# Kernel optimization log

Hardware: AMD Instinct MI355X
Metric: run time of the kernel (lower is better)

## Reference

```python
import jax, jax.numpy as jnp
import numpy as np
import math


def _lsq(x, s, bit, all_positive):
    # LSQ fake-quant: scale -> clamp -> round (STE) -> dequant
    if all_positive:
        qn, qp = 0.0, float(2 ** bit - 1)
    else:
        qn, qp = -float(2 ** (bit - 1)), float(2 ** (bit - 1) - 1)
    g = 1.0 / math.sqrt(x.size * qp)  # grad-scale factor (static)
    sg = s * g
    s_eff = sg + jax.lax.stop_gradient(s - sg)  # fwd = s, grad scaled by g
    xq = jnp.clip(x / s_eff, qn, qp)
    xq = xq + jax.lax.stop_gradient(jnp.round(xq) - xq)  # round with STE
    return xq * s_eff


def _conv(x, w, stride):
    return jax.lax.conv_general_dilated(
        x, w, window_strides=(stride, stride), padding='VALID',
        dimension_numbers=('NCHW', 'OIHW', 'NCHW'))


def setup_inputs() -> dict:
    key = jax.random.key(0)
    ks = jax.random.split(key, 5)
    B = 65536
    x = jax.random.normal(ks[0], (B, 1, 28, 28), dtype=jnp.float32)
    w1 = jax.random.normal(ks[1], (4, 1, 5, 5), dtype=jnp.float32) * 0.2
    w2 = jax.random.normal(ks[2], (8, 4, 3, 3), dtype=jnp.float32) * 0.2
    fc_w = jax.random.normal(ks[3], (10, 200), dtype=jnp.float32) * 0.07
    fc_b = jax.random.normal(ks[4], (10,), dtype=jnp.float32) * 0.01
    one = jnp.ones((1,), dtype=jnp.float32)
    return {"x": x, "w1": w1, "w2": w2, "fc_w": fc_w, "fc_b": fc_b,
            "s_in": one * 0.05, "s_w1": one * 0.02, "s_a1": one * 0.05,
            "s_w2": one * 0.02, "s_a2": one * 0.05, "s_fc": one * 0.02}


def reference(x, w1, w2, fc_w, fc_b, s_in, s_w1, s_a1, s_w2, s_a2, s_fc):
    x = _lsq(x, s_in, 8, False)
    x = _conv(x, _lsq(w1, s_w1, 8, False), 2)          # [B,4,12,12]
    x = jax.nn.relu(_lsq(x, s_a1, 8, True))
    x = _conv(x, _lsq(w2, s_w2, 8, False), 2)          # [B,8,5,5]
    x = jax.nn.relu(_lsq(x, s_a2, 8, True))
    x = x.reshape(x.shape[0], -1)                      # [B,200]
    return x @ _lsq(fc_w, s_fc, 8, False).T + fc_b     # [B,10]
```

## Files before the change

kernel.cpp:

```cpp
#include <hip/hip_runtime.h>
#include <math.h>

#define G  8
#define NG 8

#if __has_builtin(__builtin_amdgcn_sdot4)
__device__ __forceinline__ int dot4(unsigned a, unsigned b, int c) {
    return __builtin_amdgcn_sdot4((int)a, (int)b, c, false);
}
#else
__device__ __forceinline__ int dot4(unsigned a, unsigned b, int c) {
    c += (int)(signed char)(a & 255u)         * (int)(signed char)(b & 255u);
    c += (int)(signed char)((a >> 8) & 255u)  * (int)(signed char)((b >> 8) & 255u);
    c += (int)(signed char)((a >> 16) & 255u) * (int)(signed char)((b >> 16) & 255u);
    c += (int)(signed char)(a >> 24)          * (int)(signed char)(b >> 24);
    return c;
}
#endif

__device__ __forceinline__ float seff(float s, float gf) {
    float sg = s * gf;
    return sg + (s - sg);
}
__device__ __forceinline__ unsigned q8(float v, float s, float rs) {
    float q0 = v * rs;
    float r  = fmaf(-s, q0, v);
    float y  = fmaf(r, rs, q0);
    y = fminf(fmaxf(y, -128.f), 127.f);
    float t = y + 12582912.0f;
    return __float_as_uint(t);
}
__device__ __forceinline__ unsigned pack4(unsigned a, unsigned b, unsigned c, unsigned d) {
    return (a & 255u) | ((b & 255u) << 8) | ((c & 255u) << 16) | (d << 24);
}
__device__ __forceinline__ int mround(int acc, double r) {
    double t = fma((double)acc, r, 6755399441055744.0);
    return (int)__double_as_longlong(t);
}

extern "C" __global__ __launch_bounds__(256, 4)
void qcnn_fused(const float* __restrict__ x,  const float* __restrict__ w1,
                const float* __restrict__ w2, const float* __restrict__ fcw,
                const float* __restrict__ fcb,
                const float* __restrict__ s_in, const float* __restrict__ s_w1,
                const float* __restrict__ s_a1, const float* __restrict__ s_w2,
                const float* __restrict__ s_a2, const float* __restrict__ s_fc,
                float* __restrict__ out, int B,
                float gx, float gw1, float ga1, float gw2, float ga2, float gfc)
{
    __shared__ unsigned xs[2][G*196];
    __shared__ unsigned a1p[G*144];
    __shared__ unsigned a2p[G*50];
    __shared__ __align__(16) unsigned w1pk[4][5][4];
    __shared__ unsigned w2p[8][9];
    __shared__ unsigned fcp[10][50];
    __shared__ int K2s[8];
    __shared__ int K3s[10];
    __shared__ float fcbs[10];

    const int tid = threadIdx.x;
    const int g   = tid >> 5;
    const int t   = tid & 31;

    const float sx  = seff(s_in[0], gx);
    const float sw1 = seff(s_w1[0], gw1);
    const float sa1 = seff(s_a1[0], ga1);
    const float sw2 = seff(s_w2[0], gw2);
    const float sa2 = seff(s_a2[0], ga2);
    const float sfc = seff(s_fc[0], gfc);
    const float rsx = 1.0f / sx;
    const float rw1 = 1.0f / sw1;
    const float rw2 = 1.0f / sw2;
    const float rfc = 1.0f / sfc;
    const double r1 = (double)sx  * (double)sw1 / (double)sa1;
    const double r2 = (double)sa1 * (double)sw2 / (double)sa2;
    const double r3 = (double)sa2 * (double)sfc;

    const long long gbase = (long long)blockIdx.x * NG;

    float4 Rv0, Rv1, Rv2, Rv3, Rv4, Rv5, Rv6;
    auto stage_load = [&](long long grp) {
        const int nimg = (B - (int)(grp * G) < G) ? (B - (int)(grp * G)) : G;
        if (nimg != G) return;
        const float4* xp = (const float4*)x + grp * (long long)(G * 196);
        Rv0 = xp[tid];          Rv1 = xp[tid + 256]; Rv2 = xp[tid + 512];
        Rv3 = xp[tid + 768];    Rv4 = xp[tid + 1024];Rv5 = xp[tid + 1280];
        if (tid < 32) Rv6 = xp[tid + 1536];
    };
    auto stage_write = [&](long long grp, int buf) {
        const int nimg = (B - (int)(grp * G) < G) ? (B - (int)(grp * G)) : G;
        if (nimg <= 0) return;
        unsigned* dst = xs[buf];
        if (nimg == G) {
            float4 v;
            v = Rv0; dst[tid]        = pack4(q8(v.x,sx,rsx), q8(v.y,sx,rsx), q8(v.z,sx,rsx), q8(v.w,sx,rsx));
            v = Rv1; dst[tid + 256]  = pack4(q8(v.x,sx,rsx), q8(v.y,sx,rsx), q8(v.z,sx,rsx), q8(v.w,sx,rsx));
            v = Rv2; dst[tid + 512]  = pack4(q8(v.x,sx,rsx), q8(v.y,sx,rsx), q8(v.z,sx,rsx), q8(v.w,sx,rsx));
            v = Rv3; dst[tid + 768]  = pack4(q8(v.x,sx,rsx), q8(v.y,sx,rsx), q8(v.z,sx,rsx), q8(v.w,sx,rsx));
            v = Rv4; dst[tid + 1024] = pack4(q8(v.x,sx,rsx), q8(v.y,sx,rsx), q8(v.z,sx,rsx), q8(v.w,sx,rsx));
            v = Rv5; dst[tid + 1280] = pack4(q8(v.x,sx,rsx), q8(v.y,sx,rsx), q8(v.z,sx,rsx), q8(v.w,sx,rsx));
            if (tid < 32) {
                v = Rv6;
                dst[tid + 1536] = pack4(q8(v.x,sx,rsx), q8(v.y,sx,rsx), q8(v.z,sx,rsx), q8(v.w,sx,rsx));
            }
        } else {
            const float4* xp = (const float4*)x + grp * (long long)(G * 196);
            const int nv = nimg * 196;
            for (int i = tid; i < nv; i += 256) {
                float4 v = xp[i];
                dst[i] = pack4(q8(v.x,sx,rsx), q8(v.y,sx,rsx), q8(v.z,sx,rsx), q8(v.w,sx,rsx));
            }
        }
    };

    stage_load(gbase);

    if (tid < 80) {
        const int c = tid / 20, rem = tid % 20, ky = rem >> 2, vv = rem & 3;
        const float* wr = w1 + c*25 + ky*5;
        unsigned b[5];
        #pragma unroll
        for (int k = 0; k < 5; ++k) b[k] = q8(wr[k], sw1, rw1) & 255u;
        unsigned pk;
        if      (vv == 0) pk = b[0] | (b[1] << 8) | (b[2] << 16) | (b[3] << 24);
        else if (vv == 1) pk = b[4];
        else if (vv == 2) pk = (b[0] << 16) | (b[1] << 24);
        else              pk = b[2] | (b[3] << 8) | (b[4] << 16);
        w1pk[c][ky][vv] = pk;
    } else if (tid < 152) {
        const int d = tid - 80, oc = d / 9, tap = d % 9;
        unsigned pk = 0;
        #pragma unroll
        for (int ic = 0; ic < 4; ++ic)
            pk |= (q8(w2[oc*36 + ic*9 + tap], sw2, rw2) & 255u) << (8*ic);
        w2p[oc][tap] = pk;
    }
    if (tid < 10) fcbs[tid] = fcb[tid];
    for (int i = tid; i < 500; i += 256) {
        const int o = i / 50, kd = i % 50;
        const float* fr = fcw + o*200 + kd*4;
        unsigned pk = pack4(q8(fr[0],sfc,rfc), q8(fr[1],sfc,rfc),
                            q8(fr[2],sfc,rfc), q8(fr[3],sfc,rfc));
        fcp[o][kd] = pk;
    }
    __syncthreads();
    if (tid < 8) {
        int s = 0;
        #pragma unroll
        for (int d = 0; d < 9; ++d) s = dot4(w2p[tid][d], 0x01010101u, s);
        K2s[tid] = s << 7;
    } else if (tid < 18) {
        const int o = tid - 8;
        int s = 0;
        for (int d = 0; d < 50; ++d) s = dot4(fcp[o][d], 0x01010101u, s);
        K3s[o] = s << 7;
    }
    stage_write(gbase, 0);
    __syncthreads();

    int cur = 0;
    for (int it = 0; it < NG; ++it) {
        const long long grp = gbase + it;
        if (grp * G >= B) break;
        const int nimg = (B - (int)(grp * G) < G) ? (B - (int)(grp * G)) : G;

        if (it + 1 < NG) stage_load(grp + 1);

        if (g < nimg) {
            const int c  = t & 3;
            const int h  = (t >> 2) & 1;
            const int y0 = t >> 3;
            uint4 W[5];
            #pragma unroll
            for (int ky = 0; ky < 5; ++ky)
                W[ky] = *(const uint4*)&w1pk[c][ky][0];
            const unsigned* xb = &xs[cur][g*196];
            #pragma unroll
            for (int k = 0; k < 3; ++k) {
                const int y = y0 + 4*k;
                int acc[6] = {0,0,0,0,0,0};
                #pragma unroll
                for (int ky = 0; ky < 5; ++ky) {
                    const unsigned* rp = xb + (2*y + ky)*7 + 3*h;
                    const unsigned L0 = rp[0], L1 = rp[1], L2 = rp[2], L3 = rp[3];
                    acc[0] = dot4(L1, W[ky].y, dot4(L0, W[ky].x, acc[0]));
                    acc[1] = dot4(L1, W[ky].w, dot4(L0, W[ky].z, acc[1]));
                    acc[2] = dot4(L2, W[ky].y, dot4(L1, W[ky].x, acc[2]));
                    acc[3] = dot4(L2, W[ky].w, dot4(L1, W[ky].z, acc[3]));
                    acc[4] = dot4(L3, W[ky].y, dot4(L2, W[ky].x, acc[4]));
                    acc[5] = dot4(L3, W[ky].w, dot4(L2, W[ky].z, acc[5]));
                }
                unsigned char* dst = (unsigned char*)a1p + (g*144 + y*12 + 6*h)*4 + c;
                #pragma unroll
                for (int m = 0; m < 6; ++m) {
                    int q = mround(acc[m], r1);
                    q = min(max(q, 0), 255);
                    dst[4*m] = (unsigned char)(q - 128);
                }
            }
        }
        __syncthreads();

        for (int tau = tid; tau < G*40; tau += 256) {
            const int img = tau / 40;
            const int rem = tau - img*40;
            const int oc  = rem / 5;
            const int y   = rem - oc*5;
            if (img >= nimg) break;
            unsigned wv[9];
            #pragma unroll
            for (int d = 0; d < 9; ++d) wv[d] = w2p[oc][d];
            const int k2 = K2s[oc];
            const unsigned* base = &a1p[img*144];
            unsigned rw[3][12];
            #pragma unroll
            for (int ky = 0; ky < 3; ++ky) {
                const uint4* rp = (const uint4*)&base[(2*y + ky)*12];
                uint4 A = rp[0], Bv = rp[1], Cv = rp[2];
                rw[ky][0]=A.x;  rw[ky][1]=A.y;  rw[ky][2]=A.z;  rw[ky][3]=A.w;
                rw[ky][4]=Bv.x; rw[ky][5]=Bv.y; rw[ky][6]=Bv.z; rw[ky][7]=Bv.w;
                rw[ky][8]=Cv.x; rw[ky][9]=Cv.y; rw[ky][10]=Cv.z; rw[ky][11]=Cv.w;
            }
            unsigned char* dst = (unsigned char*)a2p + img*200 + oc*25 + y*5;
            #pragma unroll
            for (int jx = 0; jx < 5; ++jx) {
                int acc = k2;
                #pragma unroll
                for (int ky = 0; ky < 3; ++ky)
                    #pragma unroll
                    for (int kx = 0; kx < 3; ++kx)
                        acc = dot4(rw[ky][2*jx + kx], wv[ky*3 + kx], acc);
                int q = mround(acc, r2);
                q = min(max(q, 0), 255);
                dst[jx] = (unsigned char)(q - 128);
            }
        }

        if (it + 1 < NG) stage_write(grp + 1, cur ^ 1);
        __syncthreads();

        if (g < nimg && t < 30) {
            const int part = t / 10;
            const int o    = t - part*10;
            const int k0   = part * 17;
            const int nk   = (part == 2) ? 16 : 17;
            int acc = 0;
            for (int ki = 0; ki < nk; ++ki) {
                const int k = k0 + ki;
                acc = dot4(a2p[g*50 + k], fcp[o][k], acc);
            }
            const int self0 = (g & 1) * 32 + o;
            const int s1 = __shfl(acc, self0 + 10);
            const int s2 = __shfl(acc, self0 + 20);
            if (part == 0) {
                const int total = acc + s1 + s2 + K3s[o];
                const double oo = (double)total * r3 + (double)fcbs[o];
                out[(grp*G + g)*10 + o] = (float)oo;
            }
        }
        cur ^= 1;
    }
}

extern "C" void kernel_launch(void* const* d_in, const int* in_sizes, int n_in,
                              void* d_out, int out_size, void* d_ws, size_t ws_size,
                              hipStream_t stream) {
    const float* x    = (const float*)d_in[0];
    const float* w1   = (const float*)d_in[1];
    const float* w2   = (const float*)d_in[2];
    const float* fcw  = (const float*)d_in[3];
    const float* fcb  = (const float*)d_in[4];
    const float* s_in = (const float*)d_in[5];
    const float* s_w1 = (const float*)d_in[6];
    const float* s_a1 = (const float*)d_in[7];
    const float* s_w2 = (const float*)d_in[8];
    const float* s_a2 = (const float*)d_in[9];
    const float* s_fc = (const float*)d_in[10];

    const int B = in_sizes[0] / 784;
    const float gx  = (float)(1.0 / sqrt((double)B * 784.0 * 127.0));
    const float gw1 = (float)(1.0 / sqrt(100.0 * 127.0));
    const float ga1 = (float)(1.0 / sqrt((double)B * 576.0 * 255.0));
    const float gw2 = (float)(1.0 / sqrt(288.0 * 127.0));
    const float ga2 = (float)(1.0 / sqrt((double)B * 200.0 * 255.0));
    const float gfc = (float)(1.0 / sqrt(2000.0 * 127.0));

    const int imgs_per_block = G * NG;
    const int grid = (B + imgs_per_block - 1) / imgs_per_block;
    qcnn_fused<<<grid, 256, 0, stream>>>(x, w1, w2, fcw, fcb,
                                         s_in, s_w1, s_a1, s_w2, s_a2, s_fc,
                                         (float*)d_out, B,
                                         gx, gw1, ga1, gw2, ga2, gfc);
}
```

Measured before the change: 59.13 us.

## Give each image to one half-wave and replace block barriers with wave fences

The input staging and the conv2 work are remapped so that each image is handled only by its own 32-lane group. Each group loads, quantizes and stores its own image's tile. Because all data an image needs now stays inside one wavefront, the per-iteration __syncthreads calls become an inline s_waitcnt lgkmcnt(0) fence, which removes block-wide barrier stalls between stages. The risk is correctness: it relies on LDS ordering within a wave and on the compiler honouring the asm memory clobber. It also gives uneven conv2 work per lane, since only the lanes with (t&3)==0 do a second pass.

```diff
diff --git a/kernel.cpp b/kernel.cpp
--- a/kernel.cpp
+++ b/kernel.cpp
@@ -17,6 +17,10 @@
     return c;
 }
 #endif
+
+__device__ __forceinline__ void wave_fence() {
+    asm volatile("s_waitcnt lgkmcnt(0)" ::: "memory");
+}
 
 __device__ __forceinline__ float seff(float s, float gf) {
     float sg = s * gf;
@@ -80,36 +84,27 @@
 
     float4 Rv0, Rv1, Rv2, Rv3, Rv4, Rv5, Rv6;
     auto stage_load = [&](long long grp) {
-        const int nimg = (B - (int)(grp * G) < G) ? (B - (int)(grp * G)) : G;
-        if (nimg != G) return;
-        const float4* xp = (const float4*)x + grp * (long long)(G * 196);
-        Rv0 = xp[tid];          Rv1 = xp[tid + 256]; Rv2 = xp[tid + 512];
-        Rv3 = xp[tid + 768];    Rv4 = xp[tid + 1024];Rv5 = xp[tid + 1280];
-        if (tid < 32) Rv6 = xp[tid + 1536];
+        const long long img = grp * G + g;
+        if (img >= B) return;
+        const float4* xp = (const float4*)x + img * 196;
+        Rv0 = xp[t];        Rv1 = xp[t + 32];  Rv2 = xp[t + 64];
+        Rv3 = xp[t + 96];   Rv4 = xp[t + 128]; Rv5 = xp[t + 160];
+        if (t < 4) Rv6 = xp[t + 192];
     };
     auto stage_write = [&](long long grp, int buf) {
-        const int nimg = (B - (int)(grp * G) < G) ? (B - (int)(grp * G)) : G;
-        if (nimg <= 0) return;
-        unsigned* dst = xs[buf];
-        if (nimg == G) {
-            float4 v;
-            v = Rv0; dst[tid]        = pack4(q8(v.x,sx,rsx), q8(v.y,sx,rsx), q8(v.z,sx,rsx), q8(v.w,sx,rsx));
-            v = Rv1; dst[tid + 256]  = pack4(q8(v.x,sx,rsx), q8(v.y,sx,rsx), q8(v.z,sx,rsx), q8(v.w,sx,rsx));
-            v = Rv2; dst[tid + 512]  = pack4(q8(v.x,sx,rsx), q8(v.y,sx,rsx), q8(v.z,sx,rsx), q8(v.w,sx,rsx));
-            v = Rv3; dst[tid + 768]  = pack4(q8(v.x,sx,rsx), q8(v.y,sx,rsx), q8(v.z,sx,rsx), q8(v.w,sx,rsx));
-            v = Rv4; dst[tid + 1024] = pack4(q8(v.x,sx,rsx), q8(v.y,sx,rsx), q8(v.z,sx,rsx), q8(v.w,sx,rsx));
-            v = Rv5; dst[tid + 1280] = pack4(q8(v.x,sx,rsx), q8(v.y,sx,rsx), q8(v.z,sx,rsx), q8(v.w,sx,rsx));
-            if (tid < 32) {
-                v = Rv6;
-                dst[tid + 1536] = pack4(q8(v.x,sx,rsx), q8(v.y,sx,rsx), q8(v.z,sx,rsx), q8(v.w,sx,rsx));
-            }
-        } else {
-            const float4* xp = (const float4*)x + grp * (long long)(G * 196);
-            const int nv = nimg * 196;
-            for (int i = tid; i < nv; i += 256) {
-                float4 v = xp[i];
-                dst[i] = pack4(q8(v.x,sx,rsx), q8(v.y,sx,rsx), q8(v.z,sx,rsx), q8(v.w,sx,rsx));
-            }
+        const long long img = grp * G + g;
+        if (img >= B) return;
+        unsigned* dst = &xs[buf][g*196];
+        float4 v;
+        v = Rv0; dst[t]       = pack4(q8(v.x,sx,rsx), q8(v.y,sx,rsx), q8(v.z,sx,rsx), q8(v.w,sx,rsx));
+        v = Rv1; dst[t + 32]  = pack4(q8(v.x,sx,rsx), q8(v.y,sx,rsx), q8(v.z,sx,rsx), q8(v.w,sx,rsx));
+        v = Rv2; dst[t + 64]  = pack4(q8(v.x,sx,rsx), q8(v.y,sx,rsx), q8(v.z,sx,rsx), q8(v.w,sx,rsx));
+        v = Rv3; dst[t + 96]  = pack4(q8(v.x,sx,rsx), q8(v.y,sx,rsx), q8(v.z,sx,rsx), q8(v.w,sx,rsx));
+        v = Rv4; dst[t + 128] = pack4(q8(v.x,sx,rsx), q8(v.y,sx,rsx), q8(v.z,sx,rsx), q8(v.w,sx,rsx));
+        v = Rv5; dst[t + 160] = pack4(q8(v.x,sx,rsx), q8(v.y,sx,rsx), q8(v.z,sx,rsx), q8(v.w,sx,rsx));
+        if (t < 4) {
+            v = Rv6;
+            dst[t + 192] = pack4(q8(v.x,sx,rsx), q8(v.y,sx,rsx), q8(v.z,sx,rsx), q8(v.w,sx,rsx));
         }
     };
 
@@ -139,9 +134,8 @@
     for (int i = tid; i < 500; i += 256) {
         const int o = i / 50, kd = i % 50;
         const float* fr = fcw + o*200 + kd*4;
-        unsigned pk = pack4(q8(fr[0],sfc,rfc), q8(fr[1],sfc,rfc),
-                            q8(fr[2],sfc,rfc), q8(fr[3],sfc,rfc));
-        fcp[o][kd] = pk;
+        fcp[o][kd] = pack4(q8(fr[0],sfc,rfc), q8(fr[1],sfc,rfc),
+                           q8(fr[2],sfc,rfc), q8(fr[3],sfc,rfc));
     }
     __syncthreads();
     if (tid < 8) {
@@ -155,18 +149,19 @@
         for (int d = 0; d < 50; ++d) s = dot4(fcp[o][d], 0x01010101u, s);
         K3s[o] = s << 7;
     }
+    __syncthreads();
     stage_write(gbase, 0);
-    __syncthreads();
+    wave_fence();
 
     int cur = 0;
     for (int it = 0; it < NG; ++it) {
         const long long grp = gbase + it;
         if (grp * G >= B) break;
-        const int nimg = (B - (int)(grp * G) < G) ? (B - (int)(grp * G)) : G;
+        const bool act = (grp * G + g) < B;
 
         if (it + 1 < NG) stage_load(grp + 1);
 
-        if (g < nimg) {
+        if (act) {
             const int c  = t & 3;
             const int h  = (t >> 2) & 1;
             const int y0 = t >> 3;
@@ -199,47 +194,46 @@
                 }
             }
         }
-        __syncthreads();
-
-        for (int tau = tid; tau < G*40; tau += 256) {
-            const int img = tau / 40;
-            const int rem = tau - img*40;
-            const int oc  = rem / 5;
-            const int y   = rem - oc*5;
-            if (img >= nimg) break;
+        wave_fence();
+
+        if (act) {
+            const int oc = t >> 2;
             unsigned wv[9];
             #pragma unroll
             for (int d = 0; d < 9; ++d) wv[d] = w2p[oc][d];
             const int k2 = K2s[oc];
-            const unsigned* base = &a1p[img*144];
-            unsigned rw[3][12];
-            #pragma unroll
-            for (int ky = 0; ky < 3; ++ky) {
-                const uint4* rp = (const uint4*)&base[(2*y + ky)*12];
-                uint4 A = rp[0], Bv = rp[1], Cv = rp[2];
-                rw[ky][0]=A.x;  rw[ky][1]=A.y;  rw[ky][2]=A.z;  rw[ky][3]=A.w;
-                rw[ky][4]=Bv.x; rw[ky][5]=Bv.y; rw[ky][6]=Bv.z; rw[ky][7]=Bv.w;
-                rw[ky][8]=Cv.x; rw[ky][9]=Cv.y; rw[ky][10]=Cv.z; rw[ky][11]=Cv.w;
-            }
-            unsigned char* dst = (unsigned char*)a2p + img*200 + oc*25 + y*5;
-            #pragma unroll
-            for (int jx = 0; jx < 5; ++jx) {
-                int acc = k2;
-                #pragma unroll
-                for (int ky = 0; ky < 3; ++ky)
+            const unsigned* base = &a1p[g*144];
+            unsigned char* dstb = (unsigned char*)a2p + g*200 + oc*25;
+            #pragma unroll
+            for (int pass = 0; pass < 2; ++pass) {
+                const int y = pass ? 4 : (t & 3);
+                if (pass && (t & 3) != 0) break;
+                unsigned rw[3][12];
+                #pragma unroll
+                for (int ky = 0; ky < 3; ++ky) {
+                    const uint4* rp = (const uint4*)&base[(2*y + ky)*12];
+                    uint4 A = rp[0], Bv = rp[1], Cv = rp[2];
+                    rw[ky][0]=A.x;  rw[ky][1]=A.y;  rw[ky][2]=A.z;  rw[ky][3]=A.w;
+                    rw[ky][4]=Bv.x; rw[ky][5]=Bv.y; rw[ky][6]=Bv.z; rw[ky][7]=Bv.w;
+                    rw[ky][8]=Cv.x; rw[ky][9]=Cv.y; rw[ky][10]=Cv.z; rw[ky][11]=Cv.w;
+                }
+                #pragma unroll
+                for (int jx = 0; jx < 5; ++jx) {
+                    int acc = k2;
                     #pragma unroll
-                    for (int kx = 0; kx < 3; ++kx)
-                        acc = dot4(rw[ky][2*jx + kx], wv[ky*3 + kx], acc);
-                int q = mround(acc, r2);
-                q = min(max(q, 0), 255);
-                dst[jx] = (unsigned char)(q - 128);
-            }
-        }
-
-        if (it + 1 < NG) stage_write(grp + 1, cur ^ 1);
-        __syncthreads();
-
-        if (g < nimg && t < 30) {
+                    for (int ky = 0; ky < 3; ++ky)
+                        #pragma unroll
+                        for (int kx = 0; kx < 3; ++kx)
+                            acc = dot4(rw[ky][2*jx + kx], wv[ky*3 + kx], acc);
+                    int q = mround(acc, r2);
+                    q = min(max(q, 0), 255);
+                    dstb[y*5 + jx] = (unsigned char)(q - 128);
+                }
+            }
+        }
+        wave_fence();
+
+        if (act && t < 30) {
             const int part = t / 10;
             const int o    = t - part*10;
             const int k0   = part * 17;
@@ -257,6 +251,11 @@
                 const double oo = (double)total * r3 + (double)fcbs[o];
                 out[(grp*G + g)*10 + o] = (float)oo;
             }
+        }
+
+        if (it + 1 < NG) {
+            stage_write(grp + 1, cur ^ 1);
+            wave_fence();
         }
         cur ^= 1;
     }
```

After: 55.61 us (median of 2 runs). 5.9% less time.
